# Kernel optimization log

Hardware: AMD Instinct MI355X
Metric: run time of the kernel (lower is better)

The kernel has to match this reference:

```python
import jax, jax.numpy as jnp
import numpy as np
from jax import lax

WIN_SIZE = 11
SIGMA = 1.5
WEIGHTS = jnp.array([0.0448, 0.2856, 0.3001, 0.2363, 0.1333], dtype=jnp.float32)
C1 = (0.01 * 1.0) ** 2  # val_range = 1.0
C2 = (0.03 * 1.0) ** 2


def gaussian_kernel2d(kernel_size, sigma):
    g = jnp.arange(kernel_size, dtype=jnp.float32) - kernel_size // 2
    g = jnp.exp(-(g ** 2) / (2.0 * sigma ** 2))
    g = g / g.sum()
    return jnp.outer(g, g)  # [k, k]


def depthwise_conv(x, k2d):
    # x: [B, C, H, W]; same gaussian window applied per-channel (groups=C), VALID padding
    C = x.shape[1]
    w = jnp.broadcast_to(k2d, (C, 1) + k2d.shape).astype(x.dtype)
    return lax.conv_general_dilated(x, w, (1, 1), 'VALID',
                                    feature_group_count=C,
                                    dimension_numbers=('NCHW', 'OIHW', 'NCHW'))


def ssim_index(x, y, k2d, nonnegative=True):
    # returns (ss, cs) each of shape [B, C] (spatial mean, per channel)
    m1 = depthwise_conv(x, k2d)
    m2 = depthwise_conv(y, k2d)
    m12 = m1 * m2
    m1s = m1 * m1
    m2s = m2 * m2
    v1 = depthwise_conv(x * x, k2d) - m1s
    v2 = depthwise_conv(y * y, k2d) - m2s
    cov = depthwise_conv(x * y, k2d) - m12
    cs = (2.0 * cov + C2) / (v1 + v2 + C2)
    ss = (2.0 * m12 + C1) / (m1s + m2s + C1) * cs
    ss = ss.reshape(ss.shape[0], ss.shape[1], -1).mean(axis=-1)
    cs = cs.reshape(cs.shape[0], cs.shape[1], -1).mean(axis=-1)
    if nonnegative:
        ss = jnp.maximum(ss, 0.0)
        cs = jnp.maximum(cs, 0.0)
    return ss, cs


def avg_pool2(x):
    # F.avg_pool2d(kernel_size=2). Input spatial dims are even at every scale
    # (512 -> 32), so ceil_mode never pads; plain 2x2/2 mean pooling is exact.
    s = lax.reduce_window(x, jnp.array(0.0, x.dtype), lax.add,
                          (1, 1, 2, 2), (1, 1, 2, 2), 'VALID')
    return s * 0.25


def setup_inputs() -> dict:
    key = jax.random.key(0)
    k1, k2 = jax.random.split(key)
    B, C, H, W = 4, 12, 512, 512
    pred = jax.random.normal(k1, (B, C, H, W), dtype=jnp.float32)
    target = jax.random.randint(k2, (B, H, W), 0, C, dtype=jnp.int64)
    return {"pred": pred, "target": target}


def reference(pred, target):
    # MS_SSIMLoss.forward with process_input=True, nonnegative=True.
    # The per-class python loop in the original is an independent depthwise
    # computation per channel -> vectorized here as a C-channel grouped conv;
    # loss = mean over classes of (1 - mean over batch of msss) == 1 - mean(msss).
    num_classes = pred.shape[1]
    x = jax.nn.softmax(pred, axis=1)
    y = jax.nn.one_hot(target, num_classes, dtype=pred.dtype).transpose(0, 3, 1, 2)
    k2d = gaussian_kernel2d(WIN_SIZE, SIGMA)
    m = WEIGHTS.shape[0]
    vals = []
    for i in range(m):
        if i > 0:
            x = avg_pool2(x)
            y = avg_pool2(y)
        ss, cs = ssim_index(x, y, k2d, nonnegative=True)
        vals.append(cs if i + 1 < m else ss)
    stacked = jnp.stack(vals, axis=-1)  # [B, C, m]
    msss = jnp.prod(stacked ** WEIGHTS, axis=-1)  # [B, C]
    return 1.0 - msss.mean()
```

## Files before the change

### kernel.cpp

```cpp
#include <hip/hip_runtime.h>

#define NCH 12
#define NB  4
#define BC  48
#define HW0 (512 * 512)

#define GK_INIT { 0.00102840f, 0.00759863f, 0.03600078f, 0.10936081f, \
                  0.21300541f, 0.26601164f, 0.21300541f, 0.10936081f, \
                  0.03600078f, 0.00759863f, 0.00102840f }

__global__ void k_denom(const float4* __restrict__ pred, float4* __restrict__ U,
                        double* __restrict__ acc) {
    if (blockIdx.x == 0) {
        for (int t = threadIdx.x; t < 480; t += 256) acc[t] = 0.0;
    }
    int i = blockIdx.x * blockDim.x + threadIdx.x;
    if (i >= NB * (HW0 / 4)) return;
    int b = i >> 16;
    int p = i & 65535;
    const float4* base = pred + (((size_t)b * NCH) << 16) + p;
    float4 s = make_float4(0.f, 0.f, 0.f, 0.f);
#pragma unroll
    for (int c = 0; c < NCH; ++c) {
        float4 v = base[(size_t)c << 16];
        s.x += expf(v.x); s.y += expf(v.y);
        s.z += expf(v.z); s.w += expf(v.w);
    }
    float4 u;
    u.x = 1.f / s.x; u.y = 1.f / s.y; u.z = 1.f / s.z; u.w = 1.f / s.w;
    U[((size_t)b << 16) + p] = u;
}

__global__ __launch_bounds__(256, 8)
void k_ssim0(const float* __restrict__ pred, const float* __restrict__ U,
             const int* __restrict__ tgt, double* __restrict__ acc,
             float* __restrict__ Xp, unsigned short* __restrict__ Yp) {
    constexpr int SS = 43;
    constexpr int TS = 35;
    constexpr int H = 512, W = 512, OH = 502, OW = 502, tilesX = 16;
    __shared__ float sx[42 * SS + 4];
    __shared__ uint2 tm4[42 * TS];
    __shared__ unsigned long long ybits[30];
    __shared__ float red[8];

    const float gk[11] = GK_INIT;

    const int bc = blockIdx.y;
    const int tile = blockIdx.x;
    const int ty = tile / tilesX, tx = tile - ty * tilesX;
    const int oy = ty * 32, ox = tx * 32;
    const int tid = threadIdx.x;
    const bool interior = (oy + 41 < H) && (ox + 41 < W);

    const int b = bc / NCH, cls = bc - (bc / NCH) * NCH;
    const float* Pb = pred + (((size_t)b * NCH + cls) << 18);
    const float* Ub = U + ((size_t)b << 18);
    const int* Tb = tgt + ((size_t)b << 18);

    {
        int r = tid / 42, c = tid - (tid / 42) * 42;
#pragma unroll
        for (int k = 0; k < 7; ++k) {
            bool inr = (k < 6) || (tid < 228);
            int gy = oy + r, gx = ox + c;
            bool ld = inr && (interior || (gy < H && gx < W));
            float xv = 0.f;
            bool bit = false;
            if (ld) {
                int off = gy * W + gx;
                xv = expf(Pb[off]) * Ub[off];
                bit = (Tb[off] == cls);
            }
            unsigned long long mk = __ballot(bit);
            if ((tid & 63) == 0) ybits[(tid >> 6) + (k << 2)] = mk;
            if (inr) sx[r * SS + c] = xv;
            c += 4; r += 6;
            if (c >= 42) { c -= 42; r += 1; }
        }
        if (tid == 0) { ybits[28] = 0ull; ybits[29] = 0ull; }
    }
    __syncthreads();

    if (tid < 252) {
        int rr = tid / 6, s = tid - (tid / 6) * 6;
        int c0 = s * 6;
        const float* px = sx + rr * SS + c0;
        float ac0[6] = {}, ac1[6] = {}, ac2[6] = {}, ac3[6] = {};
        unsigned long long win;
        {
            int i0 = rr * 42 + c0;
            int w = i0 >> 6, sh = i0 & 63;
            unsigned long long lo = ybits[w], hi = ybits[w + 1];
            win = sh ? ((lo >> sh) | (hi << (64 - sh))) : lo;
        }
#pragma unroll
        for (int j = 0; j < 16; ++j) {
            float xv = px[j];
            float xx = xv * xv;
            bool bit = (win >> j) & 1;
            float yv = bit ? 1.f : 0.f;
            float xy = bit ? xv : 0.f;
#pragma unroll
            for (int o = 0; o < 6; ++o) {
                int kk = j - o;
                if (kk >= 0 && kk <= 10) {
                    float g = gk[kk];
                    ac0[o] = fmaf(g, xv, ac0[o]);
                    ac1[o] = fmaf(g, yv, ac1[o]);
                    ac2[o] = fmaf(g, xx, ac2[o]);
                    ac3[o] = fmaf(g, xy, ac3[o]);
                }
            }
        }
        int ob = rr * TS + c0;
#pragma unroll
        for (int o = 0; o < 6; ++o) {
            if (c0 + o < 32) {
                unsigned ua = __float_as_uint(ac0[o]);
                unsigned ub = __float_as_uint(ac1[o]);
                unsigned uc = __float_as_uint(ac2[o]);
                unsigned ud = __float_as_uint(ac3[o]);
                tm4[ob + o] = make_uint2((ua >> 16) | (ub & 0xFFFF0000u),
                                         (uc >> 16) | (ud & 0xFFFF0000u));
            }
        }
    }
    __syncthreads();

    const float C1 = 1e-4f, C2 = 9e-4f;
    const int cc = tid & 31, rg = tid >> 5, r0 = rg << 2;
    float a0[4] = {}, a1[4] = {}, a2[4] = {}, a3[4] = {};
    const int vb = r0 * TS + cc;
#pragma unroll
    for (int k = 0; k < 14; ++k) {
        uint2 tv = tm4[vb + k * TS];
        float m1v = __uint_as_float(tv.x << 16);
        float m2v = __uint_as_float(tv.x & 0xFFFF0000u);
        float xxv = __uint_as_float(tv.y << 16);
        float xyv = __uint_as_float(tv.y & 0xFFFF0000u);
#pragma unroll
        for (int j = 0; j < 4; ++j) {
            int kk = k - j;
            if (kk >= 0 && kk <= 10) {
                float g = gk[kk];
                a0[j] = fmaf(g, m1v, a0[j]);
                a1[j] = fmaf(g, m2v, a1[j]);
                a2[j] = fmaf(g, xxv, a2[j]);
                a3[j] = fmaf(g, xyv, a3[j]);
            }
        }
    }
    float cs_l = 0.f, ss_l = 0.f;
    const bool colok = (ox + cc < OW);
#pragma unroll
    for (int j = 0; j < 4; ++j) {
        if (colok && (oy + r0 + j < OH)) {
            float m1 = a0[j], m2 = a1[j];
            float sxx = a2[j], sxy_ = a3[j];
            float m11 = m1 * m1, m22 = m2 * m2, m12 = m1 * m2;
            float v1 = sxx - m11, v2 = m2 - m22, cov = sxy_ - m12;
            float d1 = m11 + m22 + C1, d2 = v1 + v2 + C2;
            float n2 = 2.f * cov + C2;
            float q = 1.f / (d1 * d2);
            cs_l = fmaf(n2 * d1, q, cs_l);
            ss_l = fmaf((2.f * m12 + C1) * n2, q, ss_l);
        }
    }

    {
        int py = tid >> 4, pxx = tid & 15;
        int s0 = (py * 2) * SS + pxx * 2;
        float xs = 0.25f * (sx[s0] + sx[s0 + 1] + sx[s0 + SS] + sx[s0 + SS + 1]);
        size_t oidx = ((size_t)bc * 256 + (oy >> 1) + py) * 256 + (ox >> 1) + pxx;
        Xp[oidx] = xs;
        int i0 = (py * 2) * 42 + pxx * 2, i1 = i0 + 42;
        unsigned c0 = (unsigned)((ybits[i0 >> 6] >> (i0 & 63)) & 1ull);
        unsigned c1 = (unsigned)((ybits[(i0 + 1) >> 6] >> ((i0 + 1) & 63)) & 1ull);
        unsigned c2 = (unsigned)((ybits[i1 >> 6] >> (i1 & 63)) & 1ull);
        unsigned c3 = (unsigned)((ybits[(i1 + 1) >> 6] >> ((i1 + 1) & 63)) & 1ull);
        Yp[oidx] = (unsigned short)((c0 + c1 + c2 + c3) << 6);
    }

    for (int off = 32; off; off >>= 1) {
        cs_l += __shfl_down(cs_l, off);
        ss_l += __shfl_down(ss_l, off);
    }
    int wv = tid >> 6, ln = tid & 63;
    if (ln == 0) { red[wv] = cs_l; red[4 + wv] = ss_l; }
    __syncthreads();
    if (tid == 0) {
        double cs_b = (double)red[0] + (double)red[1] + (double)red[2] + (double)red[3];
        double ss_b = (double)red[4] + (double)red[5] + (double)red[6] + (double)red[7];
        atomicAdd(&acc[bc], cs_b);
        atomicAdd(&acc[48 + bc], ss_b);
    }
}

template <int PIN>
__device__ __forceinline__ void ssim_tile_g(
    const float* __restrict__ Xs, const unsigned short* __restrict__ Ys,
    int H, int W, int OH, int OW, int tilesX, int tile, int bc,
    double* __restrict__ acc, int scale,
    float* sx, uint2* tm4, unsigned short* tm5, unsigned short* syu, float* red) {
    constexpr int SS = 43;
    constexpr int TS = 35;
    const float gk[11] = GK_INIT;

    const int ty = tile / tilesX, tx = tile - ty * tilesX;
    const int oy = ty * 32, ox = tx * 32;
    const int tid = threadIdx.x;
    const bool interior = (oy + 41 < H) && (ox + 41 < W);

    constexpr int SC = 1 << PIN;
    const int SW = W * SC;
    const float* Xb = Xs + (size_t)bc * H * W * SC * SC;
    const unsigned short* Yb = Ys + (size_t)bc * H * W * SC * SC;

    {
        int r = tid / 42, c = tid - (tid / 42) * 42;
#pragma unroll
        for (int k = 0; k < 7; ++k) {
            bool inr = (k < 6) || (tid < 228);
            int gy = oy + r, gx = ox + c;
            bool ld = inr && (interior || (gy < H && gx < W));
            float xv = 0.f;
            unsigned short yv = 0;
            if (ld) {
                if constexpr (PIN == 0) {
                    int off = gy * SW + gx;
                    xv = Xb[off];
                    yv = Yb[off];
                } else {
                    const float* q = Xb + (SC * gy) * SW + SC * gx;
                    const unsigned short* qy = Yb + (SC * gy) * SW + SC * gx;
                    float s = 0.f; unsigned us = 0;
#pragma unroll
                    for (int a = 0; a < SC; ++a) {
                        const float* qr = q + a * SW;
                        const unsigned short* qyr = qy + a * SW;
                        if constexpr (PIN == 1) {
                            float2 f = *(const float2*)qr;
                            s += f.x + f.y;
                            ushort2 uy = *(const ushort2*)qyr;
                            us += (unsigned)uy.x + (unsigned)uy.y;
                        } else {
#pragma unroll
                            for (int e4 = 0; e4 < SC / 4; ++e4) {
                                float4 f = *(const float4*)(qr + e4 * 4);
                                s += (f.x + f.y) + (f.z + f.w);
                                ushort4 uy = *(const ushort4*)(qyr + e4 * 4);
                                us += ((unsigned)uy.x + (unsigned)uy.y)
                                    + ((unsigned)uy.z + (unsigned)uy.w);
                            }
                        }
                    }
                    xv = s * (1.f / (float)(SC * SC));
                    yv = (unsigned short)(us >> (2 * PIN));
                }
            }
            if (inr) { sx[r * SS + c] = xv; syu[r * SS + c] = yv; }
            c += 4; r += 6;
            if (c >= 42) { c -= 42; r += 1; }
        }
    }
    __syncthreads();

    if (tid < 252) {
        int rr = tid / 6, s = tid - (tid / 6) * 6;
        int c0 = s * 6;
        const float* px = sx + rr * SS + c0;
        const unsigned short* pyu = syu + rr * SS + c0;
        float ac0[6] = {}, ac1[6] = {}, ac2[6] = {}, ac3[6] = {}, ac4[6] = {};
#pragma unroll
        for (int j = 0; j < 16; ++j) {
            float xv = px[j];
            float xx = xv * xv;
            float yv = (float)pyu[j];
            float xy = xv * yv;
            float yy = yv * yv;
#pragma unroll
            for (int o = 0; o < 6; ++o) {
                int kk = j - o;
                if (kk >= 0 && kk <= 10) {
                    float g = gk[kk];
                    ac0[o] = fmaf(g, xv, ac0[o]);
                    ac1[o] = fmaf(g, yv, ac1[o]);
                    ac2[o] = fmaf(g, xx, ac2[o]);
                    ac3[o] = fmaf(g, xy, ac3[o]);
                    ac4[o] = fmaf(g, yy, ac4[o]);
                }
            }
        }
        int ob = rr * TS + c0;
#pragma unroll
        for (int o = 0; o < 6; ++o) {
            if (c0 + o < 32) {
                unsigned ua = __float_as_uint(ac0[o]) + 0x8000u;
                unsigned ub = __float_as_uint(ac1[o]) + 0x8000u;
                unsigned uc = __float_as_uint(ac2[o]) + 0x8000u;
                unsigned ud = __float_as_uint(ac3[o]) + 0x8000u;
                unsigned ue = __float_as_uint(ac4[o]) + 0x8000u;
                tm4[ob + o] = make_uint2((ua >> 16) | (ub & 0xFFFF0000u),
                                         (uc >> 16) | (ud & 0xFFFF0000u));
                tm5[ob + o] = (unsigned short)(ue >> 16);
            }
        }
    }
    __syncthreads();

    const float C1 = 1e-4f, C2 = 9e-4f;
    const int cc = tid & 31, rg = tid >> 5, r0 = rg << 2;
    float a0[4] = {}, a1[4] = {}, a2[4] = {}, a3[4] = {}, a4[4] = {};
    const int vb = r0 * TS + cc;
#pragma unroll
    for (int k = 0; k < 14; ++k) {
        uint2 tv = tm4[vb + k * TS];
        float t0 = __uint_as_float(tv.x << 16);
        float t1 = __uint_as_float(tv.x & 0xFFFF0000u);
        float t2 = __uint_as_float(tv.y << 16);
        float t3 = __uint_as_float(tv.y & 0xFFFF0000u);
        float t4 = __uint_as_float((unsigned)tm5[vb + k * TS] << 16);
#pragma unroll
        for (int j = 0; j < 4; ++j) {
            int kk = k - j;
            if (kk >= 0 && kk <= 10) {
                float g = gk[kk];
                a0[j] = fmaf(g, t0, a0[j]);
                a1[j] = fmaf(g, t1, a1[j]);
                a2[j] = fmaf(g, t2, a2[j]);
                a3[j] = fmaf(g, t3, a3[j]);
                a4[j] = fmaf(g, t4, a4[j]);
            }
        }
    }
    float cs_l = 0.f, ss_l = 0.f;
    const bool colok = (ox + cc < OW);
#pragma unroll
    for (int j = 0; j < 4; ++j) {
        if (colok && (oy + r0 + j < OH)) {
            float m1 = a0[j];
            float m2 = a1[j] * (1.f / 256.f);
            float sxx = a2[j];
            float sxy_ = a3[j] * (1.f / 256.f);
            float syy_ = a4[j] * (1.f / 65536.f);
            float m11 = m1 * m1, m22 = m2 * m2, m12 = m1 * m2;
            float v1 = sxx - m11, v2 = syy_ - m22, cov = sxy_ - m12;
            float d1 = m11 + m22 + C1, d2 = v1 + v2 + C2;
            float n2 = 2.f * cov + C2;
            float q = 1.f / (d1 * d2);
            cs_l = fmaf(n2 * d1, q, cs_l);
            ss_l = fmaf((2.f * m12 + C1) * n2, q, ss_l);
        }
    }

    for (int offs = 32; offs; offs >>= 1) {
        cs_l += __shfl_down(cs_l, offs);
        ss_l += __shfl_down(ss_l, offs);
    }
    int wv = tid >> 6, ln = tid & 63;
    if (ln == 0) { red[wv] = cs_l; red[4 + wv] = ss_l; }
    __syncthreads();
    if (tid == 0) {
        double cs_b = (double)red[0] + (double)red[1] + (double)red[2] + (double)red[3];
        double ss_b = (double)red[4] + (double)red[5] + (double)red[6] + (double)red[7];
        atomicAdd(&acc[scale * 96 + bc], cs_b);
        atomicAdd(&acc[scale * 96 + 48 + bc], ss_b);
    }
}

__global__ __launch_bounds__(256, 6)
void k_rest(const float* __restrict__ X1, const unsigned short* __restrict__ Y1,
            double* __restrict__ acc) {
    __shared__ float sx[42 * 43 + 4];
    __shared__ uint2 tm4[42 * 35];
    __shared__ unsigned short tm5[42 * 35];
    __shared__ unsigned short syu[42 * 43 + 4];
    __shared__ float red[8];
    const int gb = blockIdx.x;

    if (gb < 48) {
        ssim_tile_g<3>(X1, Y1, 32, 32, 22, 22, 1, 0, gb,
                       acc, 4, sx, tm4, tm5, syu, red);
    } else if (gb < 240) {
        int t = gb - 48;
        ssim_tile_g<2>(X1, Y1, 64, 64, 54, 54, 2, t & 3, t >> 2,
                       acc, 3, sx, tm4, tm5, syu, red);
    } else if (gb < 1008) {
        int t = gb - 240;
        ssim_tile_g<1>(X1, Y1, 128, 128, 118, 118, 4, t & 15, t >> 4,
                       acc, 2, sx, tm4, tm5, syu, red);
    } else {
        int t = gb - 1008;
        ssim_tile_g<0>(X1, Y1, 256, 256, 246, 246, 8, t & 63, t >> 6,
                       acc, 1, sx, tm4, tm5, syu, red);
    }
}

__global__ void k_final(const double* __restrict__ acc, float* __restrict__ out) {
    const float wts[5] = {0.0448f, 0.2856f, 0.3001f, 0.2363f, 0.1333f};
    const float cnt[5] = {252004.f, 60516.f, 13924.f, 2916.f, 484.f};
    int tid = threadIdx.x;
    float msss = 0.f;
    if (tid < BC) {
        msss = 1.f;
#pragma unroll
        for (int s = 0; s < 5; ++s) {
            double a = (s < 4) ? acc[s * 96 + tid] : acc[s * 96 + 48 + tid];
            float v = fmaxf((float)(a / (double)cnt[s]), 0.f);
            msss *= powf(v, wts[s]);
        }
    }
    for (int off = 32; off; off >>= 1) msss += __shfl_down(msss, off);
    if (tid == 0) out[0] = 1.f - msss * (1.f / (float)BC);
}

extern "C" void kernel_launch(void* const* d_in, const int* in_sizes, int n_in,
                              void* d_out, int out_size, void* d_ws, size_t ws_size,
                              hipStream_t stream) {
    const float* pred = (const float*)d_in[0];
    const int*   tgt  = (const int*)d_in[1];
    float* out = (float*)d_out;

    double* acc = (double*)d_ws;
    float* U  = (float*)(acc + 480);
    float* X1 = U + (size_t)NB * 512 * 512;
    unsigned short* Y1 = (unsigned short*)(X1 + (size_t)BC * 256 * 256);

    k_denom<<<(NB * (HW0 / 4) + 255) / 256, 256, 0, stream>>>(
        (const float4*)pred, (float4*)U, acc);

    k_ssim0<<<dim3(256, BC), 256, 0, stream>>>(pred, U, tgt, acc, X1, Y1);

    k_rest<<<dim3(4080), 256, 0, stream>>>(X1, Y1, acc);

    k_final<<<1, 64, 0, stream>>>(acc, out);
}
```

Before: 252.6 us.

## Precompute pooled pyramids in a separate kernel and use fast exp

Adds a k_pool kernel that builds the scale-2/3/4 pooled X and Y images from the scale-1 buffers once. k_rest then reads those pyramids directly instead of re-pooling up to 8x8 source pixels per halo element. This removes redundant gathers across overlapping halo tiles, at the cost of an extra launch and extra global writes. The change also switches expf to __expf in the softmax kernels and lowers the occupancy hint on k_rest.

Result: slower. 266.7 us (+5.6%).

```diff
diff --git a/kernel.cpp b/kernel.cpp
--- a/kernel.cpp
+++ b/kernel.cpp
@@ -23,8 +23,8 @@
 #pragma unroll
     for (int c = 0; c < NCH; ++c) {
         float4 v = base[(size_t)c << 16];
-        s.x += expf(v.x); s.y += expf(v.y);
-        s.z += expf(v.z); s.w += expf(v.w);
+        s.x += __expf(v.x); s.y += __expf(v.y);
+        s.z += __expf(v.z); s.w += __expf(v.w);
     }
     float4 u;
     u.x = 1.f / s.x; u.y = 1.f / s.y; u.z = 1.f / s.z; u.w = 1.f / s.w;
@@ -68,7 +68,7 @@
             bool bit = false;
             if (ld) {
                 int off = gy * W + gx;
-                xv = expf(Pb[off]) * Ub[off];
+                xv = __expf(Pb[off]) * Ub[off];
                 bit = (Tb[off] == cls);
             }
             unsigned long long mk = __ballot(bit);
@@ -196,25 +196,71 @@
     }
 }
 
-template <int PIN>
-__device__ __forceinline__ void ssim_tile_g(
+template <int L>
+__device__ __forceinline__ void pool_one(const float* __restrict__ X1,
+                                         const unsigned short* __restrict__ Y1,
+                                         float* __restrict__ XO,
+                                         unsigned short* __restrict__ YO, int i) {
+    constexpr int SC = 1 << (L - 1);
+    const int bc = i >> (18 - 2 * L);
+    const int rem = i & ((1 << (18 - 2 * L)) - 1);
+    const int oy = rem >> (9 - L);
+    const int ox = rem & ((1 << (9 - L)) - 1);
+    const float* xb = X1 + ((size_t)bc << 16) + (oy * SC) * 256 + ox * SC;
+    const unsigned short* yb = Y1 + ((size_t)bc << 16) + (oy * SC) * 256 + ox * SC;
+    float s = 0.f; unsigned us = 0;
+#pragma unroll
+    for (int a = 0; a < SC; ++a) {
+        const float* xr = xb + a * 256;
+        const unsigned short* yr = yb + a * 256;
+        if constexpr (SC == 2) {
+            float2 f = *(const float2*)xr;
+            s += f.x + f.y;
+            ushort2 u2 = *(const ushort2*)yr;
+            us += (unsigned)u2.x + (unsigned)u2.y;
+        } else {
+#pragma unroll
+            for (int e = 0; e < SC / 4; ++e) {
+                float4 f = *(const float4*)(xr + 4 * e);
+                s += (f.x + f.y) + (f.z + f.w);
+                ushort4 u4 = *(const ushort4*)(yr + 4 * e);
+                us += ((unsigned)u4.x + (unsigned)u4.y)
+                    + ((unsigned)u4.z + (unsigned)u4.w);
+            }
+        }
+    }
+    XO[i] = s * (1.f / (float)(SC * SC));
+    YO[i] = (unsigned short)(us >> (2 * (L - 1)));
+}
+
+__global__ __launch_bounds__(256)
+void k_pool(const float* __restrict__ X1, const unsigned short* __restrict__ Y1,
+            float* __restrict__ X2, unsigned short* __restrict__ Y2,
+            float* __restrict__ X3, unsigned short* __restrict__ Y3,
+            float* __restrict__ X4, unsigned short* __restrict__ Y4) {
+    int g = blockIdx.x * 256 + threadIdx.x;
+    if (g < 786432)       pool_one<2>(X1, Y1, X2, Y2, g);
+    else if (g < 983040)  pool_one<3>(X1, Y1, X3, Y3, g - 786432);
+    else                  pool_one<4>(X1, Y1, X4, Y4, g - 983040);
+}
+
+__device__ __forceinline__ void ssim_tile(
     const float* __restrict__ Xs, const unsigned short* __restrict__ Ys,
-    int H, int W, int OH, int OW, int tilesX, int tile, int bc,
+    int H, int OH, int txs, int tile, int bc,
     double* __restrict__ acc, int scale,
     float* sx, uint2* tm4, unsigned short* tm5, unsigned short* syu, float* red) {
     constexpr int SS = 43;
     constexpr int TS = 35;
     const float gk[11] = GK_INIT;
 
-    const int ty = tile / tilesX, tx = tile - ty * tilesX;
+    const int W = H;
+    const int ty = tile >> txs, tx = tile & ((1 << txs) - 1);
     const int oy = ty * 32, ox = tx * 32;
     const int tid = threadIdx.x;
     const bool interior = (oy + 41 < H) && (ox + 41 < W);
 
-    constexpr int SC = 1 << PIN;
-    const int SW = W * SC;
-    const float* Xb = Xs + (size_t)bc * H * W * SC * SC;
-    const unsigned short* Yb = Ys + (size_t)bc * H * W * SC * SC;
+    const float* Xb = Xs + (size_t)bc * H * W;
+    const unsigned short* Yb = Ys + (size_t)bc * H * W;
 
     {
         int r = tid / 42, c = tid - (tid / 42) * 42;
@@ -226,37 +272,9 @@
             float xv = 0.f;
             unsigned short yv = 0;
             if (ld) {
-                if constexpr (PIN == 0) {
-                    int off = gy * SW + gx;
-                    xv = Xb[off];
-                    yv = Yb[off];
-                } else {
-                    const float* q = Xb + (SC * gy) * SW + SC * gx;
-                    const unsigned short* qy = Yb + (SC * gy) * SW + SC * gx;
-                    float s = 0.f; unsigned us = 0;
-#pragma unroll
-                    for (int a = 0; a < SC; ++a) {
-                        const float* qr = q + a * SW;
-                        const unsigned short* qyr = qy + a * SW;
-                        if constexpr (PIN == 1) {
-                            float2 f = *(const float2*)qr;
-                            s += f.x + f.y;
-                            ushort2 uy = *(const ushort2*)qyr;
-                            us += (unsigned)uy.x + (unsigned)uy.y;
-                        } else {
-#pragma unroll
-                            for (int e4 = 0; e4 < SC / 4; ++e4) {
-                                float4 f = *(const float4*)(qr + e4 * 4);
-                                s += (f.x + f.y) + (f.z + f.w);
-                                ushort4 uy = *(const ushort4*)(qyr + e4 * 4);
-                                us += ((unsigned)uy.x + (unsigned)uy.y)
-                                    + ((unsigned)uy.z + (unsigned)uy.w);
-                            }
-                        }
-                    }
-                    xv = s * (1.f / (float)(SC * SC));
-                    yv = (unsigned short)(us >> (2 * PIN));
-                }
+                int off = gy * W + gx;
+                xv = Xb[off];
+                yv = Yb[off];
             }
             if (inr) { sx[r * SS + c] = xv; syu[r * SS + c] = yv; }
             c += 4; r += 6;
@@ -334,7 +352,7 @@
         }
     }
     float cs_l = 0.f, ss_l = 0.f;
-    const bool colok = (ox + cc < OW);
+    const bool colok = (ox + cc < OH);
 #pragma unroll
     for (int j = 0; j < 4; ++j) {
         if (colok && (oy + r0 + j < OH)) {
@@ -368,8 +386,11 @@
     }
 }
 
-__global__ __launch_bounds__(256, 6)
+__global__ __launch_bounds__(256, 4)
 void k_rest(const float* __restrict__ X1, const unsigned short* __restrict__ Y1,
+            const float* __restrict__ X2, const unsigned short* __restrict__ Y2,
+            const float* __restrict__ X3, const unsigned short* __restrict__ Y3,
+            const float* __restrict__ X4, const unsigned short* __restrict__ Y4,
             double* __restrict__ acc) {
     __shared__ float sx[42 * 43 + 4];
     __shared__ uint2 tm4[42 * 35];
@@ -378,22 +399,17 @@
     __shared__ float red[8];
     const int gb = blockIdx.x;
 
-    if (gb < 48) {
-        ssim_tile_g<3>(X1, Y1, 32, 32, 22, 22, 1, 0, gb,
-                       acc, 4, sx, tm4, tm5, syu, red);
-    } else if (gb < 240) {
-        int t = gb - 48;
-        ssim_tile_g<2>(X1, Y1, 64, 64, 54, 54, 2, t & 3, t >> 2,
-                       acc, 3, sx, tm4, tm5, syu, red);
-    } else if (gb < 1008) {
-        int t = gb - 240;
-        ssim_tile_g<1>(X1, Y1, 128, 128, 118, 118, 4, t & 15, t >> 4,
-                       acc, 2, sx, tm4, tm5, syu, red);
-    } else {
-        int t = gb - 1008;
-        ssim_tile_g<0>(X1, Y1, 256, 256, 246, 246, 8, t & 63, t >> 6,
-                       acc, 1, sx, tm4, tm5, syu, red);
-    }
+    const float* Xs; const unsigned short* Ys;
+    int H, OH, txs, tile, bc, scale;
+    if (gb >= 1008)     { Xs = X1; Ys = Y1; H = 256; OH = 246; txs = 3;
+                          int t = gb - 1008; tile = t & 63; bc = t >> 6; scale = 1; }
+    else if (gb >= 240) { Xs = X2; Ys = Y2; H = 128; OH = 118; txs = 2;
+                          int t = gb - 240; tile = t & 15; bc = t >> 4; scale = 2; }
+    else if (gb >= 48)  { Xs = X3; Ys = Y3; H = 64;  OH = 54;  txs = 1;
+                          int t = gb - 48; tile = t & 3; bc = t >> 2; scale = 3; }
+    else                { Xs = X4; Ys = Y4; H = 32;  OH = 22;  txs = 0;
+                          tile = 0; bc = gb; scale = 4; }
+    ssim_tile(Xs, Ys, H, OH, txs, tile, bc, acc, scale, sx, tm4, tm5, syu, red);
 }
 
 __global__ void k_final(const double* __restrict__ acc, float* __restrict__ out) {
@@ -423,15 +439,23 @@
 
     double* acc = (double*)d_ws;
     float* U  = (float*)(acc + 480);
-    float* X1 = U + (size_t)NB * 512 * 512;
-    unsigned short* Y1 = (unsigned short*)(X1 + (size_t)BC * 256 * 256);
+    float* X1 = U + (size_t)NB * HW0;
+    float* X2 = X1 + (size_t)BC * 65536;
+    float* X3 = X2 + (size_t)BC * 16384;
+    float* X4 = X3 + (size_t)BC * 4096;
+    unsigned short* Y1 = (unsigned short*)(X4 + (size_t)BC * 1024);
+    unsigned short* Y2 = Y1 + (size_t)BC * 65536;
+    unsigned short* Y3 = Y2 + (size_t)BC * 16384;
+    unsigned short* Y4 = Y3 + (size_t)BC * 4096;
 
     k_denom<<<(NB * (HW0 / 4) + 255) / 256, 256, 0, stream>>>(
         (const float4*)pred, (float4*)U, acc);
 
     k_ssim0<<<dim3(256, BC), 256, 0, stream>>>(pred, U, tgt, acc, X1, Y1);
 
-    k_rest<<<dim3(4080), 256, 0, stream>>>(X1, Y1, acc);
+    k_pool<<<4032, 256, 0, stream>>>(X1, Y1, X2, Y2, X3, Y3, X4, Y4);
+
+    k_rest<<<4080, 256, 0, stream>>>(X1, Y1, X2, Y2, X3, Y3, X4, Y4, acc);
 
     k_final<<<1, 64, 0, stream>>>(acc, out);
 }
```

## Precompute bf16 softmax and class bitmask, pool all scales from full-res

Applied to the files above, without the earlier changes.

The prep kernel now computes the full softmax and stores it as bf16, along with a per-pixel 12-bit one-hot class mask. The previous version stored only the reciprocal denominator, and the scale-0 kernel recomputed exp per tile and wrote a pooled half-resolution buffer. All coarser scales now pool directly from the full-resolution bf16 and mask data, which removes the pooled intermediate and the per-tile exp and target comparison. The trade-offs are reduced precision of the softmax values and more reads per pixel for the coarse scales, which now gather up to 16x16 source pixels per sample.

Result: slower. 340.8 us (+34.9%).

```diff
diff --git a/kernel.cpp b/kernel.cpp
--- a/kernel.cpp
+++ b/kernel.cpp
@@ -9,8 +9,10 @@
                   0.21300541f, 0.26601164f, 0.21300541f, 0.10936081f, \
                   0.03600078f, 0.00759863f, 0.00102840f }
 
-__global__ void k_denom(const float4* __restrict__ pred, float4* __restrict__ U,
-                        double* __restrict__ acc) {
+__global__ __launch_bounds__(256)
+void k_prep(const float4* __restrict__ pred, const int4* __restrict__ tgt,
+            ushort4* __restrict__ X0, ushort4* __restrict__ Y0m,
+            double* __restrict__ acc) {
     if (blockIdx.x == 0) {
         for (int t = threadIdx.x; t < 480; t += 256) acc[t] = 0.0;
     }
@@ -19,22 +21,35 @@
     int b = i >> 16;
     int p = i & 65535;
     const float4* base = pred + (((size_t)b * NCH) << 16) + p;
+    float4 e[NCH];
     float4 s = make_float4(0.f, 0.f, 0.f, 0.f);
 #pragma unroll
     for (int c = 0; c < NCH; ++c) {
         float4 v = base[(size_t)c << 16];
-        s.x += expf(v.x); s.y += expf(v.y);
-        s.z += expf(v.z); s.w += expf(v.w);
+        e[c].x = __expf(v.x); e[c].y = __expf(v.y);
+        e[c].z = __expf(v.z); e[c].w = __expf(v.w);
+        s.x += e[c].x; s.y += e[c].y; s.z += e[c].z; s.w += e[c].w;
     }
     float4 u;
     u.x = 1.f / s.x; u.y = 1.f / s.y; u.z = 1.f / s.z; u.w = 1.f / s.w;
-    U[((size_t)b << 16) + p] = u;
+#pragma unroll
+    for (int c = 0; c < NCH; ++c) {
+        unsigned ax = (__float_as_uint(e[c].x * u.x) + 0x8000u) >> 16;
+        unsigned ay = (__float_as_uint(e[c].y * u.y) + 0x8000u) >> 16;
+        unsigned az = (__float_as_uint(e[c].z * u.z) + 0x8000u) >> 16;
+        unsigned aw = (__float_as_uint(e[c].w * u.w) + 0x8000u) >> 16;
+        X0[(((size_t)b * NCH + c) << 16) + p] =
+            make_ushort4((ushort)ax, (ushort)ay, (ushort)az, (ushort)aw);
+    }
+    int4 t4 = tgt[((size_t)b << 16) + p];
+    Y0m[((size_t)b << 16) + p] =
+        make_ushort4((ushort)(1u << t4.x), (ushort)(1u << t4.y),
+                     (ushort)(1u << t4.z), (ushort)(1u << t4.w));
 }
 
 __global__ __launch_bounds__(256, 8)
-void k_ssim0(const float* __restrict__ pred, const float* __restrict__ U,
-             const int* __restrict__ tgt, double* __restrict__ acc,
-             float* __restrict__ Xp, unsigned short* __restrict__ Yp) {
+void k_ssim0(const ushort* __restrict__ X0, const ushort* __restrict__ Y0m,
+             double* __restrict__ acc) {
     constexpr int SS = 43;
     constexpr int TS = 35;
     constexpr int H = 512, W = 512, OH = 502, OW = 502, tilesX = 16;
@@ -53,9 +68,8 @@
     const bool interior = (oy + 41 < H) && (ox + 41 < W);
 
     const int b = bc / NCH, cls = bc - (bc / NCH) * NCH;
-    const float* Pb = pred + (((size_t)b * NCH + cls) << 18);
-    const float* Ub = U + ((size_t)b << 18);
-    const int* Tb = tgt + ((size_t)b << 18);
+    const ushort* Xb = X0 + ((size_t)bc << 18);
+    const ushort* Mb = Y0m + ((size_t)b << 18);
 
     {
         int r = tid / 42, c = tid - (tid / 42) * 42;
@@ -68,8 +82,8 @@
             bool bit = false;
             if (ld) {
                 int off = gy * W + gx;
-                xv = expf(Pb[off]) * Ub[off];
-                bit = (Tb[off] == cls);
+                xv = __uint_as_float((unsigned)Xb[off] << 16);
+                bit = (Mb[off] >> cls) & 1;
             }
             unsigned long long mk = __ballot(bit);
             if ((tid & 63) == 0) ybits[(tid >> 6) + (k << 2)] = mk;
@@ -167,20 +181,6 @@
         }
     }
 
-    {
-        int py = tid >> 4, pxx = tid & 15;
-        int s0 = (py * 2) * SS + pxx * 2;
-        float xs = 0.25f * (sx[s0] + sx[s0 + 1] + sx[s0 + SS] + sx[s0 + SS + 1]);
-        size_t oidx = ((size_t)bc * 256 + (oy >> 1) + py) * 256 + (ox >> 1) + pxx;
-        Xp[oidx] = xs;
-        int i0 = (py * 2) * 42 + pxx * 2, i1 = i0 + 42;
-        unsigned c0 = (unsigned)((ybits[i0 >> 6] >> (i0 & 63)) & 1ull);
-        unsigned c1 = (unsigned)((ybits[(i0 + 1) >> 6] >> ((i0 + 1) & 63)) & 1ull);
-        unsigned c2 = (unsigned)((ybits[i1 >> 6] >> (i1 & 63)) & 1ull);
-        unsigned c3 = (unsigned)((ybits[(i1 + 1) >> 6] >> ((i1 + 1) & 63)) & 1ull);
-        Yp[oidx] = (unsigned short)((c0 + c1 + c2 + c3) << 6);
-    }
-
     for (int off = 32; off; off >>= 1) {
         cs_l += __shfl_down(cs_l, off);
         ss_l += __shfl_down(ss_l, off);
@@ -197,24 +197,26 @@
 }
 
 template <int PIN>
-__device__ __forceinline__ void ssim_tile_g(
-    const float* __restrict__ Xs, const unsigned short* __restrict__ Ys,
-    int H, int W, int OH, int OW, int tilesX, int tile, int bc,
-    double* __restrict__ acc, int scale,
-    float* sx, uint2* tm4, unsigned short* tm5, unsigned short* syu, float* red) {
+__device__ __forceinline__ void ssim_tile_b(
+    const ushort* __restrict__ X0, const ushort* __restrict__ Y0m,
+    int tile, int bc, double* __restrict__ acc,
+    float* sx, uint2* tm4, ushort* tm5, ushort* syu, float* red) {
     constexpr int SS = 43;
     constexpr int TS = 35;
+    constexpr int SC = 1 << PIN;
+    constexpr int H = 512 >> PIN;
+    constexpr int OH = H - 10;
+    constexpr int txs = (PIN == 1) ? 3 : (PIN == 2) ? 2 : (PIN == 3) ? 1 : 0;
     const float gk[11] = GK_INIT;
 
-    const int ty = tile / tilesX, tx = tile - ty * tilesX;
+    const int ty = tile >> txs, tx = tile & ((1 << txs) - 1);
     const int oy = ty * 32, ox = tx * 32;
     const int tid = threadIdx.x;
-    const bool interior = (oy + 41 < H) && (ox + 41 < W);
-
-    constexpr int SC = 1 << PIN;
-    const int SW = W * SC;
-    const float* Xb = Xs + (size_t)bc * H * W * SC * SC;
-    const unsigned short* Yb = Ys + (size_t)bc * H * W * SC * SC;
+    const bool interior = (oy + 41 < H) && (ox + 41 < H);
+
+    const int b = bc / NCH, cls = bc - (bc / NCH) * NCH;
+    const ushort* Xb = X0 + ((size_t)bc << 18);
+    const ushort* Mb = Y0m + ((size_t)b << 18);
 
     {
         int r = tid / 42, c = tid - (tid / 42) * 42;
@@ -222,41 +224,39 @@
         for (int k = 0; k < 7; ++k) {
             bool inr = (k < 6) || (tid < 228);
             int gy = oy + r, gx = ox + c;
-            bool ld = inr && (interior || (gy < H && gx < W));
+            bool ld = inr && (interior || (gy < H && gx < H));
             float xv = 0.f;
-            unsigned short yv = 0;
+            ushort yv = 0;
             if (ld) {
-                if constexpr (PIN == 0) {
-                    int off = gy * SW + gx;
-                    xv = Xb[off];
-                    yv = Yb[off];
-                } else {
-                    const float* q = Xb + (SC * gy) * SW + SC * gx;
-                    const unsigned short* qy = Yb + (SC * gy) * SW + SC * gx;
-                    float s = 0.f; unsigned us = 0;
-#pragma unroll
-                    for (int a = 0; a < SC; ++a) {
-                        const float* qr = q + a * SW;
-                        const unsigned short* qyr = qy + a * SW;
-                        if constexpr (PIN == 1) {
-                            float2 f = *(const float2*)qr;
-                            s += f.x + f.y;
-                            ushort2 uy = *(const ushort2*)qyr;
-                            us += (unsigned)uy.x + (unsigned)uy.y;
-                        } else {
-#pragma unroll
-                            for (int e4 = 0; e4 < SC / 4; ++e4) {
-                                float4 f = *(const float4*)(qr + e4 * 4);
-                                s += (f.x + f.y) + (f.z + f.w);
-                                ushort4 uy = *(const ushort4*)(qyr + e4 * 4);
-                                us += ((unsigned)uy.x + (unsigned)uy.y)
-                                    + ((unsigned)uy.z + (unsigned)uy.w);
-                            }
+                const ushort* qx = Xb + (SC * gy) * 512 + SC * gx;
+                const ushort* qm = Mb + (SC * gy) * 512 + SC * gx;
+                float s = 0.f; unsigned cnt = 0;
+#pragma unroll
+                for (int a = 0; a < SC; ++a) {
+                    const ushort* qxr = qx + a * 512;
+                    const ushort* qmr = qm + a * 512;
+                    if constexpr (SC == 2) {
+                        ushort2 x2 = *(const ushort2*)qxr;
+                        s += __uint_as_float((unsigned)x2.x << 16)
+                           + __uint_as_float((unsigned)x2.y << 16);
+                        ushort2 m2_ = *(const ushort2*)qmr;
+                        cnt += ((m2_.x >> cls) & 1) + ((m2_.y >> cls) & 1);
+                    } else {
+#pragma unroll
+                        for (int e = 0; e < SC / 4; ++e) {
+                            ushort4 x4 = *(const ushort4*)(qxr + 4 * e);
+                            s += (__uint_as_float((unsigned)x4.x << 16)
+                                + __uint_as_float((unsigned)x4.y << 16))
+                               + (__uint_as_float((unsigned)x4.z << 16)
+                                + __uint_as_float((unsigned)x4.w << 16));
+                            ushort4 m4 = *(const ushort4*)(qmr + 4 * e);
+                            cnt += (((m4.x >> cls) & 1) + ((m4.y >> cls) & 1))
+                                 + (((m4.z >> cls) & 1) + ((m4.w >> cls) & 1));
                         }
                     }
-                    xv = s * (1.f / (float)(SC * SC));
-                    yv = (unsigned short)(us >> (2 * PIN));
                 }
+                xv = s * (1.f / (float)(SC * SC));
+                yv = (ushort)(cnt << (8 - 2 * PIN));
             }
             if (inr) { sx[r * SS + c] = xv; syu[r * SS + c] = yv; }
             c += 4; r += 6;
@@ -269,7 +269,7 @@
         int rr = tid / 6, s = tid - (tid / 6) * 6;
         int c0 = s * 6;
         const float* px = sx + rr * SS + c0;
-        const unsigned short* pyu = syu + rr * SS + c0;
+        const ushort* pyu = syu + rr * SS + c0;
         float ac0[6] = {}, ac1[6] = {}, ac2[6] = {}, ac3[6] = {}, ac4[6] = {};
 #pragma unroll
         for (int j = 0; j < 16; ++j) {
@@ -302,7 +302,7 @@
                 unsigned ue = __float_as_uint(ac4[o]) + 0x8000u;
                 tm4[ob + o] = make_uint2((ua >> 16) | (ub & 0xFFFF0000u),
                                          (uc >> 16) | (ud & 0xFFFF0000u));
-                tm5[ob + o] = (unsigned short)(ue >> 16);
+                tm5[ob + o] = (ushort)(ue >> 16);
             }
         }
     }
@@ -334,7 +334,7 @@
         }
     }
     float cs_l = 0.f, ss_l = 0.f;
-    const bool colok = (ox + cc < OW);
+    const bool colok = (ox + cc < OH);
 #pragma unroll
     for (int j = 0; j < 4; ++j) {
         if (colok && (oy + r0 + j < OH)) {
@@ -363,36 +363,32 @@
     if (tid == 0) {
         double cs_b = (double)red[0] + (double)red[1] + (double)red[2] + (double)red[3];
         double ss_b = (double)red[4] + (double)red[5] + (double)red[6] + (double)red[7];
-        atomicAdd(&acc[scale * 96 + bc], cs_b);
-        atomicAdd(&acc[scale * 96 + 48 + bc], ss_b);
+        atomicAdd(&acc[PIN * 96 + bc], cs_b);
+        atomicAdd(&acc[PIN * 96 + 48 + bc], ss_b);
     }
 }
 
 __global__ __launch_bounds__(256, 6)
-void k_rest(const float* __restrict__ X1, const unsigned short* __restrict__ Y1,
+void k_rest(const ushort* __restrict__ X0, const ushort* __restrict__ Y0m,
             double* __restrict__ acc) {
     __shared__ float sx[42 * 43 + 4];
     __shared__ uint2 tm4[42 * 35];
-    __shared__ unsigned short tm5[42 * 35];
-    __shared__ unsigned short syu[42 * 43 + 4];
+    __shared__ ushort tm5[42 * 35];
+    __shared__ ushort syu[42 * 43 + 4];
     __shared__ float red[8];
     const int gb = blockIdx.x;
 
     if (gb < 48) {
-        ssim_tile_g<3>(X1, Y1, 32, 32, 22, 22, 1, 0, gb,
-                       acc, 4, sx, tm4, tm5, syu, red);
+        ssim_tile_b<4>(X0, Y0m, 0, gb, acc, sx, tm4, tm5, syu, red);
     } else if (gb < 240) {
         int t = gb - 48;
-        ssim_tile_g<2>(X1, Y1, 64, 64, 54, 54, 2, t & 3, t >> 2,
-                       acc, 3, sx, tm4, tm5, syu, red);
+        ssim_tile_b<3>(X0, Y0m, t & 3, t >> 2, acc, sx, tm4, tm5, syu, red);
     } else if (gb < 1008) {
         int t = gb - 240;
-        ssim_tile_g<1>(X1, Y1, 128, 128, 118, 118, 4, t & 15, t >> 4,
-                       acc, 2, sx, tm4, tm5, syu, red);
+        ssim_tile_b<2>(X0, Y0m, t & 15, t >> 4, acc, sx, tm4, tm5, syu, red);
     } else {
         int t = gb - 1008;
-        ssim_tile_g<0>(X1, Y1, 256, 256, 246, 246, 8, t & 63, t >> 6,
-                       acc, 1, sx, tm4, tm5, syu, red);
+        ssim_tile_b<1>(X0, Y0m, t & 63, t >> 6, acc, sx, tm4, tm5, syu, red);
     }
 }
 
@@ -422,16 +418,15 @@
     float* out = (float*)d_out;
 
     double* acc = (double*)d_ws;
-    float* U  = (float*)(acc + 480);
-    float* X1 = U + (size_t)NB * 512 * 512;
-    unsigned short* Y1 = (unsigned short*)(X1 + (size_t)BC * 256 * 256);
-
-    k_denom<<<(NB * (HW0 / 4) + 255) / 256, 256, 0, stream>>>(
-        (const float4*)pred, (float4*)U, acc);
-
-    k_ssim0<<<dim3(256, BC), 256, 0, stream>>>(pred, U, tgt, acc, X1, Y1);
-
-    k_rest<<<dim3(4080), 256, 0, stream>>>(X1, Y1, acc);
+    ushort* X0  = (ushort*)(acc + 480);
+    ushort* Y0m = X0 + (size_t)BC * HW0;
+
+    k_prep<<<(NB * (HW0 / 4) + 255) / 256, 256, 0, stream>>>(
+        (const float4*)pred, (const int4*)tgt, (ushort4*)X0, (ushort4*)Y0m, acc);
+
+    k_ssim0<<<dim3(256, BC), 256, 0, stream>>>(X0, Y0m, acc);
+
+    k_rest<<<dim3(4080), 256, 0, stream>>>(X0, Y0m, acc);
 
     k_final<<<1, 64, 0, stream>>>(acc, out);
 }
```

## Compute pooled scale-1 inputs in prep kernel and co-schedule scale-0 with coarser scales

Applied to the files above, without the earlier changes.

The softmax-denominator kernel now also writes the 2x2-pooled softmax and one-hot count planes for scale 1. This removes the dependency of the coarser scales on the full-resolution SSIM kernel. The scale-0 tiles and the scale 1-4 tiles are then merged into one launch with interleaved block indices and a union of their shared-memory layouts, so the smaller, tail-heavy coarse-scale work can overlap with the large scale-0 work. The cost is that the prep kernel reads pred twice and recomputes exp, and the merged kernel runs under the union's larger shared-memory footprint and launch bounds of 6, which may lower scale-0 occupancy.

New measurement: 235.4 us. 6.8% less time.

```diff
diff --git a/kernel.cpp b/kernel.cpp
--- a/kernel.cpp
+++ b/kernel.cpp
@@ -9,44 +9,80 @@
                   0.21300541f, 0.26601164f, 0.21300541f, 0.10936081f, \
                   0.03600078f, 0.00759863f, 0.00102840f }
 
-__global__ void k_denom(const float4* __restrict__ pred, float4* __restrict__ U,
-                        double* __restrict__ acc) {
+__global__ __launch_bounds__(256)
+void k_prep(const float* __restrict__ pred, const int* __restrict__ tgt,
+            float* __restrict__ U, float* __restrict__ X1,
+            unsigned short* __restrict__ Y1, double* __restrict__ acc) {
     if (blockIdx.x == 0) {
         for (int t = threadIdx.x; t < 480; t += 256) acc[t] = 0.0;
     }
-    int i = blockIdx.x * blockDim.x + threadIdx.x;
-    if (i >= NB * (HW0 / 4)) return;
-    int b = i >> 16;
-    int p = i & 65535;
-    const float4* base = pred + (((size_t)b * NCH) << 16) + p;
-    float4 s = make_float4(0.f, 0.f, 0.f, 0.f);
+    const int blk = blockIdx.x;
+    const int b  = blk >> 8;
+    const int py = blk & 255;
+    const int px = threadIdx.x;
+    const size_t o00 = (size_t)(2 * py) * 512 + 2 * px;
+    const size_t o10 = o00 + 512;
+    const float* Pb = pred + (size_t)b * NCH * HW0;
+
+    float s00 = 0.f, s01 = 0.f, s10 = 0.f, s11 = 0.f;
 #pragma unroll
     for (int c = 0; c < NCH; ++c) {
-        float4 v = base[(size_t)c << 16];
-        s.x += expf(v.x); s.y += expf(v.y);
-        s.z += expf(v.z); s.w += expf(v.w);
-    }
-    float4 u;
-    u.x = 1.f / s.x; u.y = 1.f / s.y; u.z = 1.f / s.z; u.w = 1.f / s.w;
-    U[((size_t)b << 16) + p] = u;
-}
-
-__global__ __launch_bounds__(256, 8)
-void k_ssim0(const float* __restrict__ pred, const float* __restrict__ U,
-             const int* __restrict__ tgt, double* __restrict__ acc,
-             float* __restrict__ Xp, unsigned short* __restrict__ Yp) {
+        const float* pc = Pb + (size_t)c * HW0;
+        float2 r0 = *(const float2*)(pc + o00);
+        float2 r1 = *(const float2*)(pc + o10);
+        s00 += __expf(r0.x); s01 += __expf(r0.y);
+        s10 += __expf(r1.x); s11 += __expf(r1.y);
+    }
+    float u00 = 1.f / s00, u01 = 1.f / s01, u10 = 1.f / s10, u11 = 1.f / s11;
+    float* Ub = U + (size_t)b * HW0;
+    *(float2*)(Ub + o00) = make_float2(u00, u01);
+    *(float2*)(Ub + o10) = make_float2(u10, u11);
+
+    const int* Tb = tgt + (size_t)b * HW0;
+    int2 t0 = *(const int2*)(Tb + o00);
+    int2 t1 = *(const int2*)(Tb + o10);
+
+#pragma unroll
+    for (int c = 0; c < NCH; ++c) {
+        const float* pc = Pb + (size_t)c * HW0;
+        float2 r0 = *(const float2*)(pc + o00);
+        float2 r1 = *(const float2*)(pc + o10);
+        float xs = __expf(r0.x) * u00 + __expf(r0.y) * u01
+                 + __expf(r1.x) * u10 + __expf(r1.y) * u11;
+        size_t oidx = ((size_t)(b * NCH + c) * 256 + py) * 256 + px;
+        X1[oidx] = 0.25f * xs;
+        unsigned cnt = (unsigned)(t0.x == c) + (unsigned)(t0.y == c)
+                     + (unsigned)(t1.x == c) + (unsigned)(t1.y == c);
+        Y1[oidx] = (unsigned short)(cnt << 6);
+    }
+}
+
+union SMem {
+    struct {
+        float sx[42 * 43 + 4];
+        uint2 tm4[42 * 35];
+        unsigned long long ybits[30];
+        float red[8];
+    } s0;
+    struct {
+        float sx[42 * 43 + 4];
+        uint2 tm4[42 * 35];
+        unsigned short tm5[42 * 35];
+        unsigned short syu[42 * 43 + 4];
+        float red[8];
+    } rg;
+};
+
+__device__ __forceinline__ void ssim0_tile(
+    const float* __restrict__ pred, const float* __restrict__ U,
+    const int* __restrict__ tgt, double* __restrict__ acc,
+    int tile, int bc,
+    float* sx, uint2* tm4, unsigned long long* ybits, float* red) {
     constexpr int SS = 43;
     constexpr int TS = 35;
     constexpr int H = 512, W = 512, OH = 502, OW = 502, tilesX = 16;
-    __shared__ float sx[42 * SS + 4];
-    __shared__ uint2 tm4[42 * TS];
-    __shared__ unsigned long long ybits[30];
-    __shared__ float red[8];
-
     const float gk[11] = GK_INIT;
 
-    const int bc = blockIdx.y;
-    const int tile = blockIdx.x;
     const int ty = tile / tilesX, tx = tile - ty * tilesX;
     const int oy = ty * 32, ox = tx * 32;
     const int tid = threadIdx.x;
@@ -165,20 +201,6 @@
             cs_l = fmaf(n2 * d1, q, cs_l);
             ss_l = fmaf((2.f * m12 + C1) * n2, q, ss_l);
         }
-    }
-
-    {
-        int py = tid >> 4, pxx = tid & 15;
-        int s0 = (py * 2) * SS + pxx * 2;
-        float xs = 0.25f * (sx[s0] + sx[s0 + 1] + sx[s0 + SS] + sx[s0 + SS + 1]);
-        size_t oidx = ((size_t)bc * 256 + (oy >> 1) + py) * 256 + (ox >> 1) + pxx;
-        Xp[oidx] = xs;
-        int i0 = (py * 2) * 42 + pxx * 2, i1 = i0 + 42;
-        unsigned c0 = (unsigned)((ybits[i0 >> 6] >> (i0 & 63)) & 1ull);
-        unsigned c1 = (unsigned)((ybits[(i0 + 1) >> 6] >> ((i0 + 1) & 63)) & 1ull);
-        unsigned c2 = (unsigned)((ybits[i1 >> 6] >> (i1 & 63)) & 1ull);
-        unsigned c3 = (unsigned)((ybits[(i1 + 1) >> 6] >> ((i1 + 1) & 63)) & 1ull);
-        Yp[oidx] = (unsigned short)((c0 + c1 + c2 + c3) << 6);
     }
 
     for (int off = 32; off; off >>= 1) {
@@ -369,30 +391,43 @@
 }
 
 __global__ __launch_bounds__(256, 6)
-void k_rest(const float* __restrict__ X1, const unsigned short* __restrict__ Y1,
+void k_main(const float* __restrict__ pred, const float* __restrict__ U,
+            const int* __restrict__ tgt,
+            const float* __restrict__ X1, const unsigned short* __restrict__ Y1,
             double* __restrict__ acc) {
-    __shared__ float sx[42 * 43 + 4];
-    __shared__ uint2 tm4[42 * 35];
-    __shared__ unsigned short tm5[42 * 35];
-    __shared__ unsigned short syu[42 * 43 + 4];
-    __shared__ float red[8];
+    __shared__ SMem sm;
     const int gb = blockIdx.x;
 
-    if (gb < 48) {
-        ssim_tile_g<3>(X1, Y1, 32, 32, 22, 22, 1, 0, gb,
-                       acc, 4, sx, tm4, tm5, syu, red);
-    } else if (gb < 240) {
-        int t = gb - 48;
+    int s0_idx = -1, rest_idx = -1;
+    if (gb < 16320) {
+        int r = gb & 3, q = gb >> 2;
+        if (r == 0) rest_idx = q;
+        else        s0_idx = 3 * q + (r - 1);
+    } else {
+        s0_idx = 12240 + (gb - 16320);
+    }
+
+    if (s0_idx >= 0) {
+        ssim0_tile(pred, U, tgt, acc, s0_idx & 255, s0_idx >> 8,
+                   sm.s0.sx, sm.s0.tm4, sm.s0.ybits, sm.s0.red);
+        return;
+    }
+    const int gq = rest_idx;
+    if (gq < 48) {
+        ssim_tile_g<3>(X1, Y1, 32, 32, 22, 22, 1, 0, gq,
+                       acc, 4, sm.rg.sx, sm.rg.tm4, sm.rg.tm5, sm.rg.syu, sm.rg.red);
+    } else if (gq < 240) {
+        int t = gq - 48;
         ssim_tile_g<2>(X1, Y1, 64, 64, 54, 54, 2, t & 3, t >> 2,
-                       acc, 3, sx, tm4, tm5, syu, red);
-    } else if (gb < 1008) {
-        int t = gb - 240;
+                       acc, 3, sm.rg.sx, sm.rg.tm4, sm.rg.tm5, sm.rg.syu, sm.rg.red);
+    } else if (gq < 1008) {
+        int t = gq - 240;
         ssim_tile_g<1>(X1, Y1, 128, 128, 118, 118, 4, t & 15, t >> 4,
-                       acc, 2, sx, tm4, tm5, syu, red);
+                       acc, 2, sm.rg.sx, sm.rg.tm4, sm.rg.tm5, sm.rg.syu, sm.rg.red);
     } else {
-        int t = gb - 1008;
+        int t = gq - 1008;
         ssim_tile_g<0>(X1, Y1, 256, 256, 246, 246, 8, t & 63, t >> 6,
-                       acc, 1, sx, tm4, tm5, syu, red);
+                       acc, 1, sm.rg.sx, sm.rg.tm4, sm.rg.tm5, sm.rg.syu, sm.rg.red);
     }
 }
 
@@ -423,15 +458,12 @@
 
     double* acc = (double*)d_ws;
     float* U  = (float*)(acc + 480);
-    float* X1 = U + (size_t)NB * 512 * 512;
-    unsigned short* Y1 = (unsigned short*)(X1 + (size_t)BC * 256 * 256);
-
-    k_denom<<<(NB * (HW0 / 4) + 255) / 256, 256, 0, stream>>>(
-        (const float4*)pred, (float4*)U, acc);
-
-    k_ssim0<<<dim3(256, BC), 256, 0, stream>>>(pred, U, tgt, acc, X1, Y1);
-
-    k_rest<<<dim3(4080), 256, 0, stream>>>(X1, Y1, acc);
+    float* X1 = U + (size_t)NB * HW0;
+    unsigned short* Y1 = (unsigned short*)(X1 + (size_t)BC * 65536);
+
+    k_prep<<<1024, 256, 0, stream>>>(pred, tgt, U, X1, Y1, acc);
+
+    k_main<<<16368, 256, 0, stream>>>(pred, U, tgt, X1, Y1, acc);
 
     k_final<<<1, 64, 0, stream>>>(acc, out);
 }
```
